# Performance work log

Hardware: AMD Instinct MI355X
Metric: run time of the kernel (lower is better)

Reference implementation:

```python
import jax, jax.numpy as jnp
import numpy as np

B, PP, LP, H = 128, 1024, 128, 256  # graphs, protein atoms/graph, ligand atoms/graph, hidden
NP, NL = B * PP, B * LP


def setup_inputs() -> dict:
    key = jax.random.key(0)
    ks = jax.random.split(key, 16)
    s = 0.02
    return {
        "protein_pos": 10.0 * jax.random.normal(ks[0], (NP, 3), jnp.float32),
        "ligand_pos": 10.0 * jax.random.normal(ks[1], (NL, 3), jnp.float32),
        "protein_element": jax.random.randint(ks[2], (NP,), 0, 128),
        "protein_aa": jax.random.randint(ks[3], (NP,), 0, 32),
        "protein_is_backbone": jax.random.randint(ks[4], (NP,), 0, 2),
        "ligand_type": jax.random.randint(ks[5], (NL,), 0, 16),
        "protein_batch": jnp.repeat(jnp.arange(B), PP),  # block-contiguous segments
        "ligand_batch": jnp.repeat(jnp.arange(B), LP),
        "E_elem": s * jax.random.normal(ks[6], (128, H), jnp.float32),
        "E_aa": s * jax.random.normal(ks[7], (32, H), jnp.float32),
        "E_bb": s * jax.random.normal(ks[8], (2, H), jnp.float32),
        "E_lig": s * jax.random.normal(ks[9], (16, H), jnp.float32),
        "Wd1": s * jax.random.normal(ks[10], (H, H), jnp.float32),
        "bd1": jnp.zeros((H,), jnp.float32),
        "Wd2": s * jax.random.normal(ks[11], (H, H), jnp.float32),
        "bd2": jnp.zeros((H,), jnp.float32),
        "Wa1": s * jax.random.normal(ks[12], (2 * H + 2, H), jnp.float32),
        "ba1": jnp.zeros((H,), jnp.float32),
        "Wa2": s * jax.random.normal(ks[13], (H, 1), jnp.float32),
        "ba2": jnp.zeros((1,), jnp.float32),
    }


def _pool_by_batch(x, batch, bsz):
    # mean-pool rows of x into bsz segments (index_add_ + bincount in torch)
    summed = jax.ops.segment_sum(x, batch, num_segments=bsz)
    counts = jax.ops.segment_sum(jnp.ones((x.shape[0],), x.dtype), batch, num_segments=bsz)
    return summed / jnp.maximum(counts, 1.0)[:, None]


def reference(protein_pos, ligand_pos, protein_element, protein_aa, protein_is_backbone,
              ligand_type, protein_batch, ligand_batch,
              E_elem, E_aa, E_bb, E_lig, Wd1, bd1, Wd2, bd2, Wa1, ba1, Wa2, ba2):
    # protein / ligand node embeddings
    h_protein = E_elem[protein_element] + E_aa[protein_aa] + E_bb[protein_is_backbone]
    h_ligand = E_lig[ligand_type]

    # compose_context: protein first, then ligand (mask_ligand = [0]*NP + [1]*NL)
    h_ctx = jnp.concatenate([h_protein, h_ligand], axis=0)

    # stub denoiser: pointwise 2-layer SiLU MLP producing out['h']
    h_out = jax.nn.silu(h_ctx @ Wd1 + bd1) @ Wd2 + bd2
    protein_h = h_out[:protein_pos.shape[0]]
    ligand_h = h_out[protein_pos.shape[0]:]

    pooled_protein = _pool_by_batch(protein_h, protein_batch, B)  # [B, H]
    pooled_ligand = _pool_by_batch(ligand_h, ligand_batch, B)     # [B, H]

    # contact features: per-graph cdist(lig, prot), min over protein atoms,
    # then mean & min over ligand atoms. Uniform block layout -> dense reshape.
    prot = protein_pos.reshape(B, PP, 3)
    lig = ligand_pos.reshape(B, LP, 3)
    d2 = jnp.sum((lig[:, :, None, :] - prot[:, None, :, :]) ** 2, axis=-1)  # [B, LP, PP]
    dist = jnp.sqrt(d2)
    min_lp = dist.min(axis=2)                                    # [B, LP]
    contact = jnp.stack([min_lp.mean(axis=1), min_lp.min(axis=1)], axis=-1)  # [B, 2]

    graph_feat = jnp.concatenate([pooled_protein, pooled_ligand, contact], axis=-1)  # [B, 2H+2]
    affinity = (jax.nn.silu(graph_feat @ Wa1 + ba1) @ Wa2 + ba2).squeeze(-1)  # [B]
    return affinity
```

## Files before the change

kernel.cpp:

```cpp
#include <hip/hip_runtime.h>
#include <hip/hip_bf16.h>

typedef unsigned short u16;
typedef _Float16 f16;
typedef _Float16 h8 __attribute__((ext_vector_type(8)));
typedef float f32x4 __attribute__((ext_vector_type(4)));

#define B_   128
#define PP_  1024
#define LP_  128
#define H_   256
#define NP_  131072
#define NL_  16384
#define NT_  4608
#define GRID_MLP 512
#define ASTRIDE 264

__global__ void __launch_bounds__(256) prep_k(
    const float* __restrict__ W1,
    const float* __restrict__ Ee, const float* __restrict__ Ea,
    const float* __restrict__ Eb, const float* __restrict__ El,
    f16* __restrict__ w1t, f16* __restrict__ tbl, float* __restrict__ ysum)
{
  __shared__ float t1[32][33];
  const int bid = blockIdx.x, tid = threadIdx.x;
  ysum[bid * 256 + tid] = 0.f;
  if (bid < 64) {
    const int bx = (bid & 7) * 32, by = (bid >> 3) * 32;
    const int lx = tid & 31, ly = tid >> 5;
#pragma unroll
    for (int r = 0; r < 32; r += 8)
      t1[ly + r][lx] = W1[(by + ly + r) * 256 + bx + lx];
    __syncthreads();
#pragma unroll
    for (int r = 0; r < 32; r += 8)
      w1t[(bx + ly + r) * 256 + by + lx] = (f16)t1[lx][ly + r];
  } else if (bid < 242) {
    const int idx = (bid - 64) * 256 + tid;
    float v;
    if (idx < 32768)      v = Ee[idx];
    else if (idx < 40960) v = Ea[idx - 32768];
    else if (idx < 41472) v = Eb[idx - 40960];
    else                  v = El[idx - 41472];
    tbl[idx] = (f16)v;
  }
}

__global__ void __launch_bounds__(256) prep2_k(
    const float* __restrict__ W2, const float* __restrict__ Wa1,
    const float* __restrict__ ba1, const float* __restrict__ bd2,
    float* __restrict__ wc, float* __restrict__ cvec)
{
  __shared__ float wrow[256];
  const int bid = blockIdx.x, tid = threadIdx.x;
  if (bid < 256) {
    wrow[tid] = W2[bid * 256 + tid];
    __syncthreads();
    float aP0 = 0.f, aP1 = 0.f, aL0 = 0.f, aL1 = 0.f;
#pragma unroll 4
    for (int n = 0; n < 256; n += 2) {
      float w0 = wrow[n], w1 = wrow[n + 1];
      aP0 += w0 * Wa1[n * 256 + tid];
      aP1 += w1 * Wa1[(n + 1) * 256 + tid];
      aL0 += w0 * Wa1[(256 + n) * 256 + tid];
      aL1 += w1 * Wa1[(257 + n) * 256 + tid];
    }
    wc[bid * 256 + tid]         = (aP0 + aP1) * (1.f / (float)PP_);
    wc[65536 + bid * 256 + tid] = (aL0 + aL1) * (1.f / (float)LP_);
  } else {
    float a = ba1[tid];
#pragma unroll 8
    for (int n = 0; n < 256; ++n)
      a += bd2[n] * (Wa1[n * 256 + tid] + Wa1[(256 + n) * 256 + tid]);
    cvec[tid] = a;
  }
}

__global__ void __launch_bounds__(256, 2) mlp1pool_k(
    const int* __restrict__ pel, const int* __restrict__ paa,
    const int* __restrict__ pbb, const int* __restrict__ ltyp,
    const f16* __restrict__ tbl, const f16* __restrict__ w1t,
    const float* __restrict__ bd1, float* __restrict__ ysum)
{
  __shared__ __attribute__((aligned(16))) f16 ldsA[2][32 * ASTRIDE];
  const f16* Te = tbl;
  const f16* Ta = tbl + 32768;
  const f16* Tb = tbl + 40960;
  const f16* Tl = tbl + 41472;

  const int tid = threadIdx.x;
  const int wave = tid >> 6, lane = tid & 63;
  const int l15 = lane & 15, quad = lane >> 4;
  const int n0 = wave * 64;
  const int srow = tid >> 3, scp = tid & 7;

  h8 Breg[32];
#pragma unroll
  for (int t = 0; t < 4; ++t)
#pragma unroll
    for (int ks = 0; ks < 8; ++ks)
      Breg[t * 8 + ks] = *(const h8*)(w1t + (n0 + t * 16 + l15) * 256 + ks * 32 + quad * 8);

  float bias[4];
#pragma unroll
  for (int t = 0; t < 4; ++t) bias[t] = bd1[n0 + t * 16 + l15];

  f32x4 acc[8];
#pragma unroll
  for (int i = 0; i < 8; ++i) acc[i] = (f32x4){0.f, 0.f, 0.f, 0.f};

  auto fetchv = [&](int T, h8* v) {
    if (T < 4096) {
      const int grow = T * 32 + srow;
      const h8* s0 = (const h8*)(Te + pel[grow] * 256 + scp * 32);
      const h8* s1 = (const h8*)(Ta + paa[grow] * 256 + scp * 32);
      const h8* s2 = (const h8*)(Tb + pbb[grow] * 256 + scp * 32);
#pragma unroll
      for (int c = 0; c < 4; ++c) v[c] = s0[c] + s1[c] + s2[c];
    } else {
      const int lrow = (T - 4096) * 32 + srow;
      const h8* s0 = (const h8*)(Tl + ltyp[lrow] * 256 + scp * 32);
#pragma unroll
      for (int c = 0; c < 4; ++c) v[c] = s0[c];
    }
  };

  h8 v[4];
  fetchv(blockIdx.x, v);
#pragma unroll
  for (int c = 0; c < 4; ++c)
    *(h8*)(ldsA[0] + srow * ASTRIDE + scp * 32 + c * 8) = v[c];

  int buf = 0;
  for (int T = blockIdx.x; T < NT_; T += GRID_MLP, buf ^= 1) {
    const bool prot = T < 4096;
    const int Tn = T + GRID_MLP;
    const bool more = Tn < NT_;
    __syncthreads();

    h8 vn[4];
    if (more) fetchv(Tn, vn);

#pragma unroll
    for (int ks = 0; ks < 8; ++ks) {
      h8 a0 = *(const h8*)(ldsA[buf] + l15 * ASTRIDE + ks * 32 + quad * 8);
      h8 a1 = *(const h8*)(ldsA[buf] + (16 + l15) * ASTRIDE + ks * 32 + quad * 8);
#pragma unroll
      for (int t = 0; t < 4; ++t) {
        acc[t]     = __builtin_amdgcn_mfma_f32_16x16x32_f16(a0, Breg[t * 8 + ks], acc[t], 0, 0, 0);
        acc[4 + t] = __builtin_amdgcn_mfma_f32_16x16x32_f16(a1, Breg[t * 8 + ks], acc[4 + t], 0, 0, 0);
      }
    }

    if (more) {
#pragma unroll
      for (int c = 0; c < 4; ++c)
        *(h8*)(ldsA[buf ^ 1] + srow * ASTRIDE + scp * 32 + c * 8) = vn[c];
    }

    const int batch = prot ? (T >> 5) : ((T - 4096) >> 2);
    float* pool = ysum + (prot ? 0 : 32768) + batch * 256;
#pragma unroll
    for (int t = 0; t < 4; ++t) {
      float s = 0.f;
#pragma unroll
      for (int mi = 0; mi < 2; ++mi)
#pragma unroll
        for (int r = 0; r < 4; ++r) {
          float pre = acc[mi * 4 + t][r] + bias[t];
          s += pre * __builtin_amdgcn_rcpf(1.f + __expf(-pre));
        }
      s += __shfl_xor(s, 16);
      s += __shfl_xor(s, 32);
      if (lane < 16) atomicAdd(pool + n0 + t * 16 + lane, s);
      acc[t] = (f32x4){0.f, 0.f, 0.f, 0.f};
      acc[4 + t] = (f32x4){0.f, 0.f, 0.f, 0.f};
    }
  }
}

__global__ void __launch_bounds__(512) head_k(
    const float* __restrict__ ppos, const float* __restrict__ lpos,
    const float* __restrict__ ysum, const float* __restrict__ wc,
    const float* __restrict__ cvec, const float* __restrict__ Wa1,
    const float* __restrict__ Wa2, const float* __restrict__ ba2,
    float* __restrict__ out)
{
  __shared__ float px[4 * 264], py[4 * 264], pz[4 * 264];
  __shared__ float ysc[512];
  __shared__ float part[512];
  __shared__ float lmin[128];
  __shared__ float cls[2];
  __shared__ float red[4];
  const int b = blockIdx.x, tid = threadIdx.x;

#pragma unroll
  for (int r = 0; r < 2; ++r) {
    const int i = r * 512 + tid;
    const int d = (i >> 8) * 264 + (i & 255);
    const float* p = ppos + ((size_t)b * PP_ + i) * 3;
    px[d] = p[0]; py[d] = p[1]; pz[d] = p[2];
  }
  ysc[tid] = (tid < 256) ? ysum[b * 256 + tid]
                         : ysum[32768 + b * 256 + (tid - 256)];
  __syncthreads();

  {
    const int lig = tid >> 2, prt = tid & 3;
    const float* lp = lpos + ((size_t)b * LP_ + lig) * 3;
    const float lx = lp[0], ly = lp[1], lz = lp[2];
    const float4* X4 = (const float4*)(px + prt * 264);
    const float4* Y4 = (const float4*)(py + prt * 264);
    const float4* Z4 = (const float4*)(pz + prt * 264);
    float m = 3.4e38f;
#pragma unroll 8
    for (int i = 0; i < 64; ++i) {
      float4 X = X4[i], Y = Y4[i], Z = Z4[i];
      float dx, dy, dz, d2;
      dx = lx - X.x; dy = ly - Y.x; dz = lz - Z.x;
      d2 = dx * dx + dy * dy + dz * dz; m = fminf(m, d2);
      dx = lx - X.y; dy = ly - Y.y; dz = lz - Z.y;
      d2 = dx * dx + dy * dy + dz * dz; m = fminf(m, d2);
      dx = lx - X.z; dy = ly - Y.z; dz = lz - Z.z;
      d2 = dx * dx + dy * dy + dz * dz; m = fminf(m, d2);
      dx = lx - X.w; dy = ly - Y.w; dz = lz - Z.w;
      d2 = dx * dx + dy * dy + dz * dz; m = fminf(m, d2);
    }
    m = fminf(m, __shfl_xor(m, 1));
    m = fminf(m, __shfl_xor(m, 2));
    if (prt == 0) lmin[lig] = sqrtf(m);
  }
  __syncthreads();
  if (tid < 64) {
    const float a0 = lmin[tid], a1 = lmin[tid + 64];
    float s = a0 + a1, mn = fminf(a0, a1);
#pragma unroll
    for (int off = 32; off; off >>= 1) {
      s += __shfl_down(s, off);
      mn = fminf(mn, __shfl_down(mn, off));
    }
    if (tid == 0) { cls[0] = s * (1.f / (float)LP_); cls[1] = mn; }
  }

  {
    const int g = tid >> 8, j = tid & 255;
    const float* W = wc + g * 65536 + j;
    const float* ys = ysc + g * 256;
    float a0 = 0.f, a1 = 0.f, a2 = 0.f, a3 = 0.f;
#pragma unroll 4
    for (int k = 0; k < 256; k += 4) {
      a0 += ys[k]     * W[(k)     * 256];
      a1 += ys[k + 1] * W[(k + 1) * 256];
      a2 += ys[k + 2] * W[(k + 2) * 256];
      a3 += ys[k + 3] * W[(k + 3) * 256];
    }
    part[tid] = (a0 + a1) + (a2 + a3);
  }
  __syncthreads();

  if (tid < 256) {
    float pre = part[tid] + part[256 + tid] + cvec[tid]
              + cls[0] * Wa1[512 * 256 + tid] + cls[1] * Wa1[513 * 256 + tid];
    float s = pre * __builtin_amdgcn_rcpf(1.f + __expf(-pre));
    float p = s * Wa2[tid];
#pragma unroll
    for (int off = 32; off; off >>= 1) p += __shfl_down(p, off);
    if ((tid & 63) == 0) red[tid >> 6] = p;
  }
  __syncthreads();
  if (tid == 0) out[b] = (red[0] + red[1]) + (red[2] + red[3]) + ba2[0];
}

extern "C" void kernel_launch(void* const* d_in, const int* in_sizes, int n_in,
                              void* d_out, int out_size, void* d_ws, size_t ws_size,
                              hipStream_t stream)
{
  const float* protein_pos = (const float*)d_in[0];
  const float* ligand_pos  = (const float*)d_in[1];
  const int*   pel  = (const int*)d_in[2];
  const int*   paa  = (const int*)d_in[3];
  const int*   pbb  = (const int*)d_in[4];
  const int*   ltyp = (const int*)d_in[5];
  const float* Ee  = (const float*)d_in[8];
  const float* Ea  = (const float*)d_in[9];
  const float* Eb  = (const float*)d_in[10];
  const float* El  = (const float*)d_in[11];
  const float* Wd1 = (const float*)d_in[12];
  const float* bd1 = (const float*)d_in[13];
  const float* Wd2 = (const float*)d_in[14];
  const float* bd2 = (const float*)d_in[15];
  const float* Wa1 = (const float*)d_in[16];
  const float* ba1 = (const float*)d_in[17];
  const float* Wa2 = (const float*)d_in[18];
  const float* ba2 = (const float*)d_in[19];
  float* out = (float*)d_out;

  char* ws = (char*)d_ws;
  f16*   w1t  = (f16*)(ws);
  f16*   tbl  = (f16*)(ws + 131072);
  float* ysum = (float*)(ws + 262144);
  float* wc   = (float*)(ws + 524288);
  float* cvec = (float*)(ws + 1048576);

  prep_k<<<256, 256, 0, stream>>>(Wd1, Ee, Ea, Eb, El, w1t, tbl, ysum);
  prep2_k<<<257, 256, 0, stream>>>(Wd2, Wa1, ba1, bd2, wc, cvec);
  mlp1pool_k<<<GRID_MLP, 256, 0, stream>>>(pel, paa, pbb, ltyp, tbl, w1t, bd1, ysum);
  head_k<<<B_, 512, 0, stream>>>(protein_pos, ligand_pos, ysum, wc, cvec,
                                 Wa1, Wa2, ba2, out);
}
```

Before: 158.9 us.

## Merge prep kernels, batch-aligned MLP tiles with register pooling, widen head kernel

Merges the two prep kernels into a single launch, which drops one kernel launch. The MLP kernel now uses 1152 blocks with 9 blocks per graph, each processing 4 fixed 32-row tiles. It folds the bias into the accumulator init and sums pooled values in registers, so it issues one set of atomics per block instead of one per tile. The head kernel goes to 1024 threads, splitting the contact search 8 ways and the wc matvec 4 ways for more parallelism per graph. The risks are the ligand-pooling predicate (s>=5) needing to be exactly right, and the higher per-block thread count in the head.

```diff
diff --git a/kernel.cpp b/kernel.cpp
--- a/kernel.cpp
+++ b/kernel.cpp
@@ -12,49 +12,44 @@
 #define H_   256
 #define NP_  131072
 #define NL_  16384
-#define NT_  4608
-#define GRID_MLP 512
 #define ASTRIDE 264
 
-__global__ void __launch_bounds__(256) prep_k(
+__global__ void __launch_bounds__(256) prep_m(
     const float* __restrict__ W1,
     const float* __restrict__ Ee, const float* __restrict__ Ea,
     const float* __restrict__ Eb, const float* __restrict__ El,
-    f16* __restrict__ w1t, f16* __restrict__ tbl, float* __restrict__ ysum)
+    const float* __restrict__ W2, const float* __restrict__ Wa1,
+    const float* __restrict__ ba1, const float* __restrict__ bd2,
+    f16* __restrict__ w1t, f16* __restrict__ tbl, float* __restrict__ ysum,
+    float* __restrict__ wc, float* __restrict__ cvec)
 {
   __shared__ float t1[32][33];
-  const int bid = blockIdx.x, tid = threadIdx.x;
-  ysum[bid * 256 + tid] = 0.f;
-  if (bid < 64) {
-    const int bx = (bid & 7) * 32, by = (bid >> 3) * 32;
-    const int lx = tid & 31, ly = tid >> 5;
-#pragma unroll
-    for (int r = 0; r < 32; r += 8)
-      t1[ly + r][lx] = W1[(by + ly + r) * 256 + bx + lx];
-    __syncthreads();
-#pragma unroll
-    for (int r = 0; r < 32; r += 8)
-      w1t[(bx + ly + r) * 256 + by + lx] = (f16)t1[lx][ly + r];
-  } else if (bid < 242) {
-    const int idx = (bid - 64) * 256 + tid;
-    float v;
-    if (idx < 32768)      v = Ee[idx];
-    else if (idx < 40960) v = Ea[idx - 32768];
-    else if (idx < 41472) v = Eb[idx - 40960];
-    else                  v = El[idx - 41472];
-    tbl[idx] = (f16)v;
-  }
-}
-
-__global__ void __launch_bounds__(256) prep2_k(
-    const float* __restrict__ W2, const float* __restrict__ Wa1,
-    const float* __restrict__ ba1, const float* __restrict__ bd2,
-    float* __restrict__ wc, float* __restrict__ cvec)
-{
   __shared__ float wrow[256];
   const int bid = blockIdx.x, tid = threadIdx.x;
   if (bid < 256) {
-    wrow[tid] = W2[bid * 256 + tid];
+    ysum[bid * 256 + tid] = 0.f;
+    if (bid < 64) {
+      const int bx = (bid & 7) * 32, by = (bid >> 3) * 32;
+      const int lx = tid & 31, ly = tid >> 5;
+#pragma unroll
+      for (int r = 0; r < 32; r += 8)
+        t1[ly + r][lx] = W1[(by + ly + r) * 256 + bx + lx];
+      __syncthreads();
+#pragma unroll
+      for (int r = 0; r < 32; r += 8)
+        w1t[(bx + ly + r) * 256 + by + lx] = (f16)t1[lx][ly + r];
+    } else if (bid < 242) {
+      const int idx = (bid - 64) * 256 + tid;
+      float v;
+      if (idx < 32768)      v = Ee[idx];
+      else if (idx < 40960) v = Ea[idx - 32768];
+      else if (idx < 41472) v = Eb[idx - 40960];
+      else                  v = El[idx - 41472];
+      tbl[idx] = (f16)v;
+    }
+  } else if (bid < 512) {
+    const int r = bid - 256;
+    wrow[tid] = W2[r * 256 + tid];
     __syncthreads();
     float aP0 = 0.f, aP1 = 0.f, aL0 = 0.f, aL1 = 0.f;
 #pragma unroll 4
@@ -65,8 +60,8 @@
       aL0 += w0 * Wa1[(256 + n) * 256 + tid];
       aL1 += w1 * Wa1[(257 + n) * 256 + tid];
     }
-    wc[bid * 256 + tid]         = (aP0 + aP1) * (1.f / (float)PP_);
-    wc[65536 + bid * 256 + tid] = (aL0 + aL1) * (1.f / (float)LP_);
+    wc[r * 256 + tid]         = (aP0 + aP1) * (1.f / (float)PP_);
+    wc[65536 + r * 256 + tid] = (aL0 + aL1) * (1.f / (float)LP_);
   } else {
     float a = ba1[tid];
 #pragma unroll 8
@@ -93,6 +88,7 @@
   const int l15 = lane & 15, quad = lane >> 4;
   const int n0 = wave * 64;
   const int srow = tid >> 3, scp = tid & 7;
+  const int batch = blockIdx.x / 9, s = blockIdx.x % 9;
 
   h8 Breg[32];
 #pragma unroll
@@ -105,20 +101,19 @@
 #pragma unroll
   for (int t = 0; t < 4; ++t) bias[t] = bd1[n0 + t * 16 + l15];
 
-  f32x4 acc[8];
-#pragma unroll
-  for (int i = 0; i < 8; ++i) acc[i] = (f32x4){0.f, 0.f, 0.f, 0.f};
-
-  auto fetchv = [&](int T, h8* v) {
-    if (T < 4096) {
-      const int grow = T * 32 + srow;
+  float accP[4] = {0.f, 0.f, 0.f, 0.f};
+  float accL[4] = {0.f, 0.f, 0.f, 0.f};
+
+  auto fetchv = [&](int li, h8* v) {
+    if (li < 32) {
+      const int grow = batch * PP_ + li * 32 + srow;
       const h8* s0 = (const h8*)(Te + pel[grow] * 256 + scp * 32);
       const h8* s1 = (const h8*)(Ta + paa[grow] * 256 + scp * 32);
       const h8* s2 = (const h8*)(Tb + pbb[grow] * 256 + scp * 32);
 #pragma unroll
       for (int c = 0; c < 4; ++c) v[c] = s0[c] + s1[c] + s2[c];
     } else {
-      const int lrow = (T - 4096) * 32 + srow;
+      const int lrow = batch * LP_ + (li - 32) * 32 + srow;
       const h8* s0 = (const h8*)(Tl + ltyp[lrow] * 256 + scp * 32);
 #pragma unroll
       for (int c = 0; c < 4; ++c) v[c] = s0[c];
@@ -126,20 +121,27 @@
   };
 
   h8 v[4];
-  fetchv(blockIdx.x, v);
+  fetchv(s, v);
 #pragma unroll
   for (int c = 0; c < 4; ++c)
     *(h8*)(ldsA[0] + srow * ASTRIDE + scp * 32 + c * 8) = v[c];
 
   int buf = 0;
-  for (int T = blockIdx.x; T < NT_; T += GRID_MLP, buf ^= 1) {
-    const bool prot = T < 4096;
-    const int Tn = T + GRID_MLP;
-    const bool more = Tn < NT_;
+#pragma unroll 1
+  for (int it = 0; it < 4; ++it, buf ^= 1) {
+    const int li = s + it * 9;
+    const bool more = it < 3;
     __syncthreads();
 
     h8 vn[4];
-    if (more) fetchv(Tn, vn);
+    if (more) fetchv(li + 9, vn);
+
+    f32x4 acc[8];
+#pragma unroll
+    for (int t = 0; t < 4; ++t) {
+      acc[t]     = (f32x4){bias[t], bias[t], bias[t], bias[t]};
+      acc[4 + t] = acc[t];
+    }
 
 #pragma unroll
     for (int ks = 0; ks < 8; ++ks) {
@@ -158,63 +160,76 @@
         *(h8*)(ldsA[buf ^ 1] + srow * ASTRIDE + scp * 32 + c * 8) = vn[c];
     }
 
-    const int batch = prot ? (T >> 5) : ((T - 4096) >> 2);
-    float* pool = ysum + (prot ? 0 : 32768) + batch * 256;
+    const bool isP = li < 32;
 #pragma unroll
     for (int t = 0; t < 4; ++t) {
-      float s = 0.f;
+      float sum = 0.f;
 #pragma unroll
       for (int mi = 0; mi < 2; ++mi)
 #pragma unroll
         for (int r = 0; r < 4; ++r) {
-          float pre = acc[mi * 4 + t][r] + bias[t];
-          s += pre * __builtin_amdgcn_rcpf(1.f + __expf(-pre));
+          float pre = acc[mi * 4 + t][r];
+          sum += pre * __builtin_amdgcn_rcpf(1.f + __expf(-pre));
         }
-      s += __shfl_xor(s, 16);
-      s += __shfl_xor(s, 32);
-      if (lane < 16) atomicAdd(pool + n0 + t * 16 + lane, s);
-      acc[t] = (f32x4){0.f, 0.f, 0.f, 0.f};
-      acc[4 + t] = (f32x4){0.f, 0.f, 0.f, 0.f};
+      if (isP) accP[t] += sum; else accL[t] += sum;
+    }
+  }
+
+  float* poolP = ysum + batch * 256;
+  float* poolL = ysum + 32768 + batch * 256;
+#pragma unroll
+  for (int t = 0; t < 4; ++t) {
+    float sp = accP[t];
+    sp += __shfl_xor(sp, 16);
+    sp += __shfl_xor(sp, 32);
+    if (lane < 16) atomicAdd(poolP + n0 + t * 16 + lane, sp);
+  }
+  if (s >= 5) {
+#pragma unroll
+    for (int t = 0; t < 4; ++t) {
+      float sl = accL[t];
+      sl += __shfl_xor(sl, 16);
+      sl += __shfl_xor(sl, 32);
+      if (lane < 16) atomicAdd(poolL + n0 + t * 16 + lane, sl);
     }
   }
 }
 
-__global__ void __launch_bounds__(512) head_k(
+__global__ void __launch_bounds__(1024) head_k(
     const float* __restrict__ ppos, const float* __restrict__ lpos,
     const float* __restrict__ ysum, const float* __restrict__ wc,
     const float* __restrict__ cvec, const float* __restrict__ Wa1,
     const float* __restrict__ Wa2, const float* __restrict__ ba2,
     float* __restrict__ out)
 {
-  __shared__ float px[4 * 264], py[4 * 264], pz[4 * 264];
+  __shared__ float px[8 * 132], py[8 * 132], pz[8 * 132];
   __shared__ float ysc[512];
-  __shared__ float part[512];
+  __shared__ float part[1024];
   __shared__ float lmin[128];
   __shared__ float cls[2];
   __shared__ float red[4];
   const int b = blockIdx.x, tid = threadIdx.x;
 
-#pragma unroll
-  for (int r = 0; r < 2; ++r) {
-    const int i = r * 512 + tid;
-    const int d = (i >> 8) * 264 + (i & 255);
-    const float* p = ppos + ((size_t)b * PP_ + i) * 3;
+  {
+    const int d = (tid >> 7) * 132 + (tid & 127);
+    const float* p = ppos + ((size_t)b * PP_ + tid) * 3;
     px[d] = p[0]; py[d] = p[1]; pz[d] = p[2];
   }
-  ysc[tid] = (tid < 256) ? ysum[b * 256 + tid]
-                         : ysum[32768 + b * 256 + (tid - 256)];
+  if (tid < 512)
+    ysc[tid] = (tid < 256) ? ysum[b * 256 + tid]
+                           : ysum[32768 + b * 256 + (tid - 256)];
   __syncthreads();
 
   {
-    const int lig = tid >> 2, prt = tid & 3;
+    const int lig = tid >> 3, prt = tid & 7;
     const float* lp = lpos + ((size_t)b * LP_ + lig) * 3;
     const float lx = lp[0], ly = lp[1], lz = lp[2];
-    const float4* X4 = (const float4*)(px + prt * 264);
-    const float4* Y4 = (const float4*)(py + prt * 264);
-    const float4* Z4 = (const float4*)(pz + prt * 264);
+    const float4* X4 = (const float4*)(px + prt * 132);
+    const float4* Y4 = (const float4*)(py + prt * 132);
+    const float4* Z4 = (const float4*)(pz + prt * 132);
     float m = 3.4e38f;
 #pragma unroll 8
-    for (int i = 0; i < 64; ++i) {
+    for (int i = 0; i < 32; ++i) {
       float4 X = X4[i], Y = Y4[i], Z = Z4[i];
       float dx, dy, dz, d2;
       dx = lx - X.x; dy = ly - Y.x; dz = lz - Z.x;
@@ -228,41 +243,45 @@
     }
     m = fminf(m, __shfl_xor(m, 1));
     m = fminf(m, __shfl_xor(m, 2));
+    m = fminf(m, __shfl_xor(m, 4));
     if (prt == 0) lmin[lig] = sqrtf(m);
   }
   __syncthreads();
   if (tid < 64) {
     const float a0 = lmin[tid], a1 = lmin[tid + 64];
-    float s = a0 + a1, mn = fminf(a0, a1);
+    float sm = a0 + a1, mn = fminf(a0, a1);
 #pragma unroll
     for (int off = 32; off; off >>= 1) {
-      s += __shfl_down(s, off);
+      sm += __shfl_down(sm, off);
       mn = fminf(mn, __shfl_down(mn, off));
     }
-    if (tid == 0) { cls[0] = s * (1.f / (float)LP_); cls[1] = mn; }
+    if (tid == 0) { cls[0] = sm * (1.f / (float)LP_); cls[1] = mn; }
   }
 
   {
     const int g = tid >> 8, j = tid & 255;
-    const float* W = wc + g * 65536 + j;
-    const float* ys = ysc + g * 256;
-    float a0 = 0.f, a1 = 0.f, a2 = 0.f, a3 = 0.f;
-#pragma unroll 4
-    for (int k = 0; k < 256; k += 4) {
-      a0 += ys[k]     * W[(k)     * 256];
-      a1 += ys[k + 1] * W[(k + 1) * 256];
-      a2 += ys[k + 2] * W[(k + 2) * 256];
-      a3 += ys[k + 3] * W[(k + 3) * 256];
-    }
-    part[tid] = (a0 + a1) + (a2 + a3);
+    const int kbase = g * 128;
+    const float* W = wc + (g >> 1) * 65536 + (kbase & 255) * 256 + j;
+    const float* ys = ysc + kbase;
+    float a[8];
+#pragma unroll
+    for (int u = 0; u < 8; ++u) a[u] = 0.f;
+#pragma unroll 2
+    for (int k = 0; k < 128; k += 8) {
+#pragma unroll
+      for (int u = 0; u < 8; ++u)
+        a[u] += ys[k + u] * W[(k + u) * 256];
+    }
+    part[tid] = ((a[0] + a[1]) + (a[2] + a[3])) + ((a[4] + a[5]) + (a[6] + a[7]));
   }
   __syncthreads();
 
   if (tid < 256) {
-    float pre = part[tid] + part[256 + tid] + cvec[tid]
+    float pre = (part[tid] + part[256 + tid]) + (part[512 + tid] + part[768 + tid])
+              + cvec[tid]
               + cls[0] * Wa1[512 * 256 + tid] + cls[1] * Wa1[513 * 256 + tid];
-    float s = pre * __builtin_amdgcn_rcpf(1.f + __expf(-pre));
-    float p = s * Wa2[tid];
+    float si = pre * __builtin_amdgcn_rcpf(1.f + __expf(-pre));
+    float p = si * Wa2[tid];
 #pragma unroll
     for (int off = 32; off; off >>= 1) p += __shfl_down(p, off);
     if ((tid & 63) == 0) red[tid >> 6] = p;
@@ -302,9 +321,9 @@
   float* wc   = (float*)(ws + 524288);
   float* cvec = (float*)(ws + 1048576);
 
-  prep_k<<<256, 256, 0, stream>>>(Wd1, Ee, Ea, Eb, El, w1t, tbl, ysum);
-  prep2_k<<<257, 256, 0, stream>>>(Wd2, Wa1, ba1, bd2, wc, cvec);
-  mlp1pool_k<<<GRID_MLP, 256, 0, stream>>>(pel, paa, pbb, ltyp, tbl, w1t, bd1, ysum);
-  head_k<<<B_, 512, 0, stream>>>(protein_pos, ligand_pos, ysum, wc, cvec,
-                                 Wa1, Wa2, ba2, out);
+  prep_m<<<513, 256, 0, stream>>>(Wd1, Ee, Ea, Eb, El, Wd2, Wa1, ba1, bd2,
+                                  w1t, tbl, ysum, wc, cvec);
+  mlp1pool_k<<<1152, 256, 0, stream>>>(pel, paa, pbb, ltyp, tbl, w1t, bd1, ysum);
+  head_k<<<B_, 1024, 0, stream>>>(protein_pos, ligand_pos, ysum, wc, cvec,
+                                  Wa1, Wa2, ba2, out);
 }
```

New measurement: 165.8 us. +4.3%, slower.

## Fold Wd1 into embedding tables, replacing per-atom GEMM with gather-sum pooling

Applied to the files above, without the earlier changes.

Because the first linear layer is applied to a sum of embeddings, each embedding table is premultiplied by Wd1, with bd1 folded into the small tables. The per-atom layer-1 preactivation then reduces to a gather and add of three pre-projected rows. The MFMA GEMM kernel is replaced by a simple gather, SiLU and pool kernel, and the two prep kernels are merged into one launch. The risk is that preactivations are now stored in fp16 after projection, which changes rounding, and the pool kernel spreads its atomics over more blocks.

```diff
diff --git a/kernel.cpp b/kernel.cpp
--- a/kernel.cpp
+++ b/kernel.cpp
@@ -1,9 +1,8 @@
 #include <hip/hip_runtime.h>
 #include <hip/hip_bf16.h>
 
-typedef unsigned short u16;
 typedef _Float16 f16;
-typedef _Float16 h8 __attribute__((ext_vector_type(8)));
+typedef _Float16 h4 __attribute__((ext_vector_type(4)));
 typedef float f32x4 __attribute__((ext_vector_type(4)));
 
 #define B_   128
@@ -12,61 +11,56 @@
 #define H_   256
 #define NP_  131072
 #define NL_  16384
-#define NT_  4608
-#define GRID_MLP 512
-#define ASTRIDE 264
+
 
 __global__ void __launch_bounds__(256) prep_k(
     const float* __restrict__ W1,
     const float* __restrict__ Ee, const float* __restrict__ Ea,
     const float* __restrict__ Eb, const float* __restrict__ El,
-    f16* __restrict__ w1t, f16* __restrict__ tbl, float* __restrict__ ysum)
-{
-  __shared__ float t1[32][33];
+    const float* __restrict__ bd1, const float* __restrict__ W2,
+    const float* __restrict__ Wa1, const float* __restrict__ ba1,
+    const float* __restrict__ bd2,
+    f16* __restrict__ tbl, float* __restrict__ wc, float* __restrict__ cvec,
+    float* __restrict__ ysum)
+{
+  __shared__ float src[256];
   const int bid = blockIdx.x, tid = threadIdx.x;
-  ysum[bid * 256 + tid] = 0.f;
-  if (bid < 64) {
-    const int bx = (bid & 7) * 32, by = (bid >> 3) * 32;
-    const int lx = tid & 31, ly = tid >> 5;
-#pragma unroll
-    for (int r = 0; r < 32; r += 8)
-      t1[ly + r][lx] = W1[(by + ly + r) * 256 + bx + lx];
+  if (bid < 256) ysum[bid * 256 + tid] = 0.f;
+
+  if (bid < 178) {
+    const float* s;
+    float badd = 0.f;
+    if (bid < 128)      s = Ee + bid * 256;
+    else if (bid < 160) s = Ea + (bid - 128) * 256;
+    else if (bid < 162) { s = Eb + (bid - 160) * 256; badd = bd1[tid]; }
+    else                { s = El + (bid - 162) * 256; badd = bd1[tid]; }
+    src[tid] = s[tid];
     __syncthreads();
-#pragma unroll
-    for (int r = 0; r < 32; r += 8)
-      w1t[(bx + ly + r) * 256 + by + lx] = (f16)t1[lx][ly + r];
-  } else if (bid < 242) {
-    const int idx = (bid - 64) * 256 + tid;
-    float v;
-    if (idx < 32768)      v = Ee[idx];
-    else if (idx < 40960) v = Ea[idx - 32768];
-    else if (idx < 41472) v = Eb[idx - 40960];
-    else                  v = El[idx - 41472];
-    tbl[idx] = (f16)v;
-  }
-}
-
-__global__ void __launch_bounds__(256) prep2_k(
-    const float* __restrict__ W2, const float* __restrict__ Wa1,
-    const float* __restrict__ ba1, const float* __restrict__ bd2,
-    float* __restrict__ wc, float* __restrict__ cvec)
-{
-  __shared__ float wrow[256];
-  const int bid = blockIdx.x, tid = threadIdx.x;
-  if (bid < 256) {
-    wrow[tid] = W2[bid * 256 + tid];
+    float a0 = 0.f, a1 = 0.f, a2 = 0.f, a3 = 0.f;
+#pragma unroll 4
+    for (int k = 0; k < 256; k += 4) {
+      a0 += src[k]     * W1[(k)     * 256 + tid];
+      a1 += src[k + 1] * W1[(k + 1) * 256 + tid];
+      a2 += src[k + 2] * W1[(k + 2) * 256 + tid];
+      a3 += src[k + 3] * W1[(k + 3) * 256 + tid];
+    }
+    tbl[bid * 256 + tid] = (f16)(((a0 + a1) + (a2 + a3)) + badd);
+  } else if (bid < 690) {
+    const int r = bid - 178;
+    const int half = r >> 8, rr = r & 255;
+    src[tid] = W2[rr * 256 + tid];
     __syncthreads();
-    float aP0 = 0.f, aP1 = 0.f, aL0 = 0.f, aL1 = 0.f;
-#pragma unroll 4
-    for (int n = 0; n < 256; n += 2) {
-      float w0 = wrow[n], w1 = wrow[n + 1];
-      aP0 += w0 * Wa1[n * 256 + tid];
-      aP1 += w1 * Wa1[(n + 1) * 256 + tid];
-      aL0 += w0 * Wa1[(256 + n) * 256 + tid];
-      aL1 += w1 * Wa1[(257 + n) * 256 + tid];
-    }
-    wc[bid * 256 + tid]         = (aP0 + aP1) * (1.f / (float)PP_);
-    wc[65536 + bid * 256 + tid] = (aL0 + aL1) * (1.f / (float)LP_);
+    const float* W = Wa1 + half * 256 * 256 + tid;
+    float a0 = 0.f, a1 = 0.f, a2 = 0.f, a3 = 0.f;
+#pragma unroll 4
+    for (int n = 0; n < 256; n += 4) {
+      a0 += src[n]     * W[(n)     * 256];
+      a1 += src[n + 1] * W[(n + 1) * 256];
+      a2 += src[n + 2] * W[(n + 2) * 256];
+      a3 += src[n + 3] * W[(n + 3) * 256];
+    }
+    const float scale = half ? (1.f / (float)LP_) : (1.f / (float)PP_);
+    wc[half * 65536 + rr * 256 + tid] = ((a0 + a1) + (a2 + a3)) * scale;
   } else {
     float a = ba1[tid];
 #pragma unroll 8
@@ -76,106 +70,53 @@
   }
 }
 
-__global__ void __launch_bounds__(256, 2) mlp1pool_k(
+__global__ void __launch_bounds__(256, 4) gpool_k(
     const int* __restrict__ pel, const int* __restrict__ paa,
     const int* __restrict__ pbb, const int* __restrict__ ltyp,
-    const f16* __restrict__ tbl, const f16* __restrict__ w1t,
-    const float* __restrict__ bd1, float* __restrict__ ysum)
-{
-  __shared__ __attribute__((aligned(16))) f16 ldsA[2][32 * ASTRIDE];
-  const f16* Te = tbl;
-  const f16* Ta = tbl + 32768;
-  const f16* Tb = tbl + 40960;
-  const f16* Tl = tbl + 41472;
-
-  const int tid = threadIdx.x;
-  const int wave = tid >> 6, lane = tid & 63;
-  const int l15 = lane & 15, quad = lane >> 4;
-  const int n0 = wave * 64;
-  const int srow = tid >> 3, scp = tid & 7;
-
-  h8 Breg[32];
-#pragma unroll
-  for (int t = 0; t < 4; ++t)
-#pragma unroll
-    for (int ks = 0; ks < 8; ++ks)
-      Breg[t * 8 + ks] = *(const h8*)(w1t + (n0 + t * 16 + l15) * 256 + ks * 32 + quad * 8);
-
-  float bias[4];
-#pragma unroll
-  for (int t = 0; t < 4; ++t) bias[t] = bd1[n0 + t * 16 + l15];
-
-  f32x4 acc[8];
-#pragma unroll
-  for (int i = 0; i < 8; ++i) acc[i] = (f32x4){0.f, 0.f, 0.f, 0.f};
-
-  auto fetchv = [&](int T, h8* v) {
-    if (T < 4096) {
-      const int grow = T * 32 + srow;
-      const h8* s0 = (const h8*)(Te + pel[grow] * 256 + scp * 32);
-      const h8* s1 = (const h8*)(Ta + paa[grow] * 256 + scp * 32);
-      const h8* s2 = (const h8*)(Tb + pbb[grow] * 256 + scp * 32);
-#pragma unroll
-      for (int c = 0; c < 4; ++c) v[c] = s0[c] + s1[c] + s2[c];
-    } else {
-      const int lrow = (T - 4096) * 32 + srow;
-      const h8* s0 = (const h8*)(Tl + ltyp[lrow] * 256 + scp * 32);
-#pragma unroll
-      for (int c = 0; c < 4; ++c) v[c] = s0[c];
-    }
-  };
-
-  h8 v[4];
-  fetchv(blockIdx.x, v);
-#pragma unroll
-  for (int c = 0; c < 4; ++c)
-    *(h8*)(ldsA[0] + srow * ASTRIDE + scp * 32 + c * 8) = v[c];
-
-  int buf = 0;
-  for (int T = blockIdx.x; T < NT_; T += GRID_MLP, buf ^= 1) {
-    const bool prot = T < 4096;
-    const int Tn = T + GRID_MLP;
-    const bool more = Tn < NT_;
-    __syncthreads();
-
-    h8 vn[4];
-    if (more) fetchv(Tn, vn);
-
-#pragma unroll
-    for (int ks = 0; ks < 8; ++ks) {
-      h8 a0 = *(const h8*)(ldsA[buf] + l15 * ASTRIDE + ks * 32 + quad * 8);
-      h8 a1 = *(const h8*)(ldsA[buf] + (16 + l15) * ASTRIDE + ks * 32 + quad * 8);
-#pragma unroll
-      for (int t = 0; t < 4; ++t) {
-        acc[t]     = __builtin_amdgcn_mfma_f32_16x16x32_f16(a0, Breg[t * 8 + ks], acc[t], 0, 0, 0);
-        acc[4 + t] = __builtin_amdgcn_mfma_f32_16x16x32_f16(a1, Breg[t * 8 + ks], acc[4 + t], 0, 0, 0);
+    const f16* __restrict__ tbl, float* __restrict__ ysum)
+{
+  const int tid = threadIdx.x, wave = tid >> 6, lane = tid & 63;
+  const int batch = blockIdx.x / 18, g = blockIdx.x % 18;
+  const int c0 = lane * 4;
+  f32x4 acc = (f32x4){0.f, 0.f, 0.f, 0.f};
+
+  if (g < 16) {
+    const int base = batch * PP_ + g * 64 + wave * 16;
+#pragma unroll 4
+    for (int r = 0; r < 16; ++r) {
+      const int idx = base + r;
+      h4 va = *(const h4*)(tbl + pel[idx] * 256 + c0);
+      h4 vb = *(const h4*)(tbl + 32768 + paa[idx] * 256 + c0);
+      h4 vc = *(const h4*)(tbl + 40960 + pbb[idx] * 256 + c0);
+#pragma unroll
+      for (int i = 0; i < 4; ++i) {
+        float pre = (float)va[i] + (float)vb[i] + (float)vc[i];
+        acc[i] += pre * __builtin_amdgcn_rcpf(1.f + __expf(-pre));
       }
     }
-
-    if (more) {
-#pragma unroll
-      for (int c = 0; c < 4; ++c)
-        *(h8*)(ldsA[buf ^ 1] + srow * ASTRIDE + scp * 32 + c * 8) = vn[c];
-    }
-
-    const int batch = prot ? (T >> 5) : ((T - 4096) >> 2);
-    float* pool = ysum + (prot ? 0 : 32768) + batch * 256;
-#pragma unroll
-    for (int t = 0; t < 4; ++t) {
-      float s = 0.f;
-#pragma unroll
-      for (int mi = 0; mi < 2; ++mi)
-#pragma unroll
-        for (int r = 0; r < 4; ++r) {
-          float pre = acc[mi * 4 + t][r] + bias[t];
-          s += pre * __builtin_amdgcn_rcpf(1.f + __expf(-pre));
-        }
-      s += __shfl_xor(s, 16);
-      s += __shfl_xor(s, 32);
-      if (lane < 16) atomicAdd(pool + n0 + t * 16 + lane, s);
-      acc[t] = (f32x4){0.f, 0.f, 0.f, 0.f};
-      acc[4 + t] = (f32x4){0.f, 0.f, 0.f, 0.f};
-    }
+  } else {
+    const int base = batch * LP_ + (g - 16) * 64 + wave * 16;
+#pragma unroll 4
+    for (int r = 0; r < 16; ++r) {
+      const int idx = base + r;
+      h4 v = *(const h4*)(tbl + 41472 + ltyp[idx] * 256 + c0);
+#pragma unroll
+      for (int i = 0; i < 4; ++i) {
+        float pre = (float)v[i];
+        acc[i] += pre * __builtin_amdgcn_rcpf(1.f + __expf(-pre));
+      }
+    }
+  }
+
+  __shared__ f32x4 red[3][64];
+  if (wave) red[wave - 1][lane] = acc;
+  __syncthreads();
+  if (wave == 0) {
+    f32x4 a1 = red[0][lane], a2 = red[1][lane], a3 = red[2][lane];
+    float* pool = ysum + (g < 16 ? 0 : 32768) + batch * 256 + c0;
+#pragma unroll
+    for (int i = 0; i < 4; ++i)
+      atomicAdd(pool + i, ((acc[i] + a1[i]) + (a2[i] + a3[i])));
   }
 }
 
@@ -213,7 +154,7 @@
     const float4* Y4 = (const float4*)(py + prt * 264);
     const float4* Z4 = (const float4*)(pz + prt * 264);
     float m = 3.4e38f;
-#pragma unroll 8
+#pragma unroll 4
     for (int i = 0; i < 64; ++i) {
       float4 X = X4[i], Y = Y4[i], Z = Z4[i];
       float dx, dy, dz, d2;
@@ -233,36 +174,37 @@
   __syncthreads();
   if (tid < 64) {
     const float a0 = lmin[tid], a1 = lmin[tid + 64];
-    float s = a0 + a1, mn = fminf(a0, a1);
+    float sm = a0 + a1, mn = fminf(a0, a1);
 #pragma unroll
     for (int off = 32; off; off >>= 1) {
-      s += __shfl_down(s, off);
+      sm += __shfl_down(sm, off);
       mn = fminf(mn, __shfl_down(mn, off));
     }
-    if (tid == 0) { cls[0] = s * (1.f / (float)LP_); cls[1] = mn; }
+    if (tid == 0) { cls[0] = sm * (1.f / (float)LP_); cls[1] = mn; }
   }
 
   {
-    const int g = tid >> 8, j = tid & 255;
-    const float* W = wc + g * 65536 + j;
-    const float* ys = ysc + g * 256;
-    float a0 = 0.f, a1 = 0.f, a2 = 0.f, a3 = 0.f;
-#pragma unroll 4
-    for (int k = 0; k < 256; k += 4) {
-      a0 += ys[k]     * W[(k)     * 256];
-      a1 += ys[k + 1] * W[(k + 1) * 256];
-      a2 += ys[k + 2] * W[(k + 2) * 256];
-      a3 += ys[k + 3] * W[(k + 3) * 256];
-    }
-    part[tid] = (a0 + a1) + (a2 + a3);
+    const int gg = tid >> 8, j = tid & 255;
+    const float* W = wc + gg * 65536 + j;
+    const float* ys = ysc + gg * 256;
+    float a[8];
+#pragma unroll
+    for (int u = 0; u < 8; ++u) a[u] = 0.f;
+#pragma unroll 2
+    for (int k = 0; k < 256; k += 8) {
+#pragma unroll
+      for (int u = 0; u < 8; ++u)
+        a[u] += ys[k + u] * W[(k + u) * 256];
+    }
+    part[tid] = ((a[0] + a[1]) + (a[2] + a[3])) + ((a[4] + a[5]) + (a[6] + a[7]));
   }
   __syncthreads();
 
   if (tid < 256) {
     float pre = part[tid] + part[256 + tid] + cvec[tid]
               + cls[0] * Wa1[512 * 256 + tid] + cls[1] * Wa1[513 * 256 + tid];
-    float s = pre * __builtin_amdgcn_rcpf(1.f + __expf(-pre));
-    float p = s * Wa2[tid];
+    float si = pre * __builtin_amdgcn_rcpf(1.f + __expf(-pre));
+    float p = si * Wa2[tid];
 #pragma unroll
     for (int off = 32; off; off >>= 1) p += __shfl_down(p, off);
     if ((tid & 63) == 0) red[tid >> 6] = p;
@@ -296,15 +238,14 @@
   float* out = (float*)d_out;
 
   char* ws = (char*)d_ws;
-  f16*   w1t  = (f16*)(ws);
-  f16*   tbl  = (f16*)(ws + 131072);
-  float* ysum = (float*)(ws + 262144);
-  float* wc   = (float*)(ws + 524288);
-  float* cvec = (float*)(ws + 1048576);
-
-  prep_k<<<256, 256, 0, stream>>>(Wd1, Ee, Ea, Eb, El, w1t, tbl, ysum);
-  prep2_k<<<257, 256, 0, stream>>>(Wd2, Wa1, ba1, bd2, wc, cvec);
-  mlp1pool_k<<<GRID_MLP, 256, 0, stream>>>(pel, paa, pbb, ltyp, tbl, w1t, bd1, ysum);
+  f16*   tbl  = (f16*)(ws);
+  float* ysum = (float*)(ws + 98304);
+  float* wc   = (float*)(ws + 360448);
+  float* cvec = (float*)(ws + 884736);
+
+  prep_k<<<691, 256, 0, stream>>>(Wd1, Ee, Ea, Eb, El, bd1, Wd2, Wa1, ba1, bd2,
+                                  tbl, wc, cvec, ysum);
+  gpool_k<<<B_ * 18, 256, 0, stream>>>(pel, paa, pbb, ltyp, tbl, ysum);
   head_k<<<B_, 512, 0, stream>>>(protein_pos, ligand_pos, ysum, wc, cvec,
                                  Wa1, Wa2, ba2, out);
 }
```

Measured after the change: 139.9 us. 1.14x faster.
